# Kernel tuning notes

Hardware: AMD Instinct MI355X
Metric: run time of the kernel (lower is better)

## Reference

```python
import jax, jax.numpy as jnp
import numpy as np

N_NODES = 50000
N_EDGES = 800000
HID = 128
OUT = 10
N_LAYERS = 3
N_GRAPHS = 64
BN_EPS = 1e-5


def setup_inputs() -> dict:
    key = jax.random.key(0)
    ks = jax.random.split(key, 12)
    x = jax.random.normal(ks[0], (N_NODES, HID), dtype=jnp.float32)
    edge_index = jax.random.randint(ks[1], (2, N_EDGES), 0, N_NODES)
    batch = jnp.sort(jax.random.randint(ks[2], (N_NODES,), 0, N_GRAPHS))
    s = 1.0 / np.sqrt(HID)
    # per-layer MLP params (in_channels == hidden_channels so all layers stack)
    W1s = jax.random.uniform(ks[3], (N_LAYERS, HID, HID), jnp.float32, -s, s)
    b1s = jax.random.uniform(ks[4], (N_LAYERS, HID), jnp.float32, -s, s)
    W2s = jax.random.uniform(ks[5], (N_LAYERS, HID, HID), jnp.float32, -s, s)
    b2s = jax.random.uniform(ks[6], (N_LAYERS, HID), jnp.float32, -s, s)
    gammas = jnp.ones((N_LAYERS, HID), jnp.float32)
    betas = jnp.zeros((N_LAYERS, HID), jnp.float32)
    Wlin = jax.random.uniform(ks[7], (HID, OUT), jnp.float32, -s, s)
    blin = jax.random.uniform(ks[8], (OUT,), jnp.float32, -s, s)
    return {"x": x, "W1s": W1s, "b1s": b1s, "W2s": W2s, "b2s": b2s,
            "gammas": gammas, "betas": betas, "Wlin": Wlin, "blin": blin,
            "edge_index": edge_index, "batch": batch}


def reference(x, W1s, b1s, W2s, b2s, gammas, betas, Wlin, blin, edge_index, batch):
    src, dst = edge_index[0], edge_index[1]
    n = x.shape[0]
    for l in range(N_LAYERS):
        # GINConv (eps=0): h_i = MLP(x_i + sum_{j->i} x_j)
        agg = jax.ops.segment_sum(x[src], dst, num_segments=n)  # [N, HID]
        h = x + agg
        h = jnp.maximum(h @ W1s[l] + b1s[l], 0.0) @ W2s[l] + b2s[l]
        # BatchNorm1d (batch statistics)
        mean = jnp.mean(h, axis=0)
        var = jnp.var(h, axis=0)
        h = (h - mean) * jax.lax.rsqrt(var + BN_EPS) * gammas[l] + betas[l]
        x = jnp.maximum(h, 0.0)  # ReLU; dropout is identity in eval mode
    # global_add_pool over graphs
    g = jax.ops.segment_sum(x, batch, num_segments=N_GRAPHS)  # [G, HID]
    return g @ Wlin + blin
```

## Files before the change

kernel.cpp:

```cpp
#include <hip/hip_runtime.h>

#define N_NODES 50000
#define N_EDGES 800000
#define HID 128
#define OUTC 10
#define N_GRAPHS 64
#define BN_EPS 1e-5f

#define MLP_BLOCKS (N_NODES / 16)

#define NB 196
#define BCAP 5632
#define EPB 2048
#define NBLK_A ((N_EDGES + EPB - 1) / EPB)

typedef __attribute__((ext_vector_type(8))) short short8_t;
typedef __attribute__((ext_vector_type(4))) float f32x4;

__device__ __forceinline__ unsigned short f2bf(float f) {
    unsigned u = __float_as_uint(f);
    u += 0x7FFFu + ((u >> 16) & 1u);
    return (unsigned short)(u >> 16);
}
__device__ __forceinline__ float bf2f(unsigned short s) {
    return __uint_as_float(((unsigned)s) << 16);
}
__device__ __forceinline__ float2 bfp2f(unsigned v) {
    float2 r;
    r.x = __uint_as_float(v << 16);
    r.y = __uint_as_float(v & 0xFFFF0000u);
    return r;
}

__global__ __launch_bounds__(256) void k_bucket(const int* __restrict__ src,
                                                const int* __restrict__ dst,
                                                int* __restrict__ bucketCnt,
                                                unsigned* __restrict__ ebuf) {
    __shared__ int cnt[NB];
    __shared__ int base[NB];
    int t = threadIdx.x;
    for (int i = t; i < NB; i += 256) cnt[i] = 0;
    __syncthreads();
    int e0 = blockIdx.x * EPB;
    int e1 = e0 + EPB; if (e1 > N_EDGES) e1 = N_EDGES;
    for (int e = e0 + t; e < e1; e += 256)
        atomicAdd(&cnt[dst[e] >> 8], 1);
    __syncthreads();
    for (int i = t; i < NB; i += 256) {
        int c = cnt[i];
        base[i] = c ? atomicAdd(&bucketCnt[i], c) : 0;
        cnt[i] = 0;
    }
    __syncthreads();
    for (int e = e0 + t; e < e1; e += 256) {
        int d = dst[e];
        int s = src[e];
        int b = d >> 8;
        int r = atomicAdd(&cnt[b], 1);
        ebuf[(size_t)b * BCAP + base[b] + r] = ((unsigned)(d & 255) << 16) | (unsigned)s;
    }
}

__global__ __launch_bounds__(256) void k_bsort(const int* __restrict__ bucketCnt,
                                               const unsigned* __restrict__ ebuf,
                                               unsigned short* __restrict__ srcSorted,
                                               int* __restrict__ estart,
                                               int* __restrict__ eend) {
    __shared__ int cnt[256];
    __shared__ int sh[256];
    __shared__ int pos[256];
    int b = blockIdx.x;
    int t = threadIdx.x;
    int n = bucketCnt[b];
    int bBase = b * BCAP;
    const unsigned* eb = ebuf + (size_t)bBase;
    cnt[t] = 0;
    __syncthreads();
    for (int i = t; i < n; i += 256) atomicAdd(&cnt[eb[i] >> 16], 1);
    __syncthreads();
    int v = cnt[t];
    sh[t] = v;
    __syncthreads();
    for (int off = 1; off < 256; off <<= 1) {
        int x = sh[t];
        if (t >= off) x += sh[t - off];
        __syncthreads();
        sh[t] = x;
        __syncthreads();
    }
    int excl = sh[t] - v;
    pos[t] = excl;
    int node = b * 256 + t;
    if (node < N_NODES) {
        estart[node] = bBase + excl;
        eend[node] = bBase + excl + v;
    }
    __syncthreads();
    for (int i = t; i < n; i += 256) {
        unsigned pe = eb[i];
        int dl = pe >> 16;
        int p = atomicAdd(&pos[dl], 1);
        srcSorted[bBase + p] = (unsigned short)(pe & 0xFFFFu);
    }
}

#define X2BF_ITEMS (N_NODES * HID / 8)
__global__ void k_prep(const float* __restrict__ x, const float* __restrict__ W1s,
                       const float* __restrict__ W2s,
                       unsigned short* __restrict__ xbf, unsigned short* __restrict__ Wp) {
    int gid = blockIdx.x * 256 + threadIdx.x;
    if (gid < X2BF_ITEMS) {
        const float4* p = (const float4*)&x[(size_t)gid * 8];
        float4 a = p[0], b = p[1];
        short8_t o = { (short)f2bf(a.x), (short)f2bf(a.y), (short)f2bf(a.z), (short)f2bf(a.w),
                       (short)f2bf(b.x), (short)f2bf(b.y), (short)f2bf(b.z), (short)f2bf(b.w) };
        *(short8_t*)&xbf[(size_t)gid * 8] = o;
    } else {
        int idx = gid - X2BF_ITEMS;
        if (idx >= 6 * 2048) return;
        int mat = idx >> 11;
        int rem = idx & 2047;
        int lane = rem & 63;
        int ks = (rem >> 6) & 3;
        int nt = rem >> 8;
        int l = mat >> 1;
        const float* W = (mat & 1) ? (W2s + (size_t)l * HID * HID) : (W1s + (size_t)l * HID * HID);
        int n = nt * 16 + (lane & 15);
        int k0 = ks * 32 + (lane >> 4) * 8;
        short8_t o;
#pragma unroll
        for (int j = 0; j < 8; j++) o[j] = (short)f2bf(W[(size_t)(k0 + j) * HID + n]);
        *(short8_t*)&Wp[(size_t)idx * 8] = o;
    }
}

#define MPITCH 136

template <bool BN>
__global__ __launch_bounds__(256) void k_aggmlp(const unsigned short* __restrict__ X,
                                                const float* __restrict__ sc,
                                                const int* __restrict__ estart,
                                                const int* __restrict__ eend,
                                                const unsigned short* __restrict__ srcSorted,
                                                const unsigned short* __restrict__ W1p,
                                                const float* __restrict__ b1,
                                                const unsigned short* __restrict__ W2p,
                                                const float* __restrict__ b2,
                                                unsigned short* __restrict__ hbf,
                                                float* __restrict__ bnpart) {
    __shared__ __align__(16) unsigned short As[16 * MPITCH];
    __shared__ __align__(16) unsigned short Ts[16 * MPITCH];

    int tid = threadIdx.x;
    int wave = tid >> 6;
    int lane = tid & 63;
    int lrow = lane & 15;
    int quad = lane >> 4;
    int half = lane >> 5;
    int hl = lane & 31;
    int hq = hl >> 4;
    int rowBase = blockIdx.x * 16;
    int col0 = lrow * 8;

    float scv[8], shv[8];
    if (BN) {
#pragma unroll
        for (int j = 0; j < 8; j++) { scv[j] = sc[col0 + j]; shv[j] = sc[HID + col0 + j]; }
    }

    for (int pr = 0; pr < 2; pr++) {
        int tr = wave * 4 + pr * 2 + half;
        int node = rowBase + tr;
        float acc[8];
        {
            short8_t ov = *(const short8_t*)&X[(size_t)node * HID + col0];
            uint4 uu = *(uint4*)&ov;
            float2 p0 = bfp2f(uu.x), p1 = bfp2f(uu.y), p2 = bfp2f(uu.z), p3 = bfp2f(uu.w);
            float f[8] = { p0.x, p0.y, p1.x, p1.y, p2.x, p2.y, p3.x, p3.y };
#pragma unroll
            for (int j = 0; j < 8; j++) {
                float v = BN ? fmaxf(f[j] * scv[j] + shv[j], 0.f) : f[j];
                acc[j] = (hq == 0) ? v : 0.f;
            }
        }

        int e0 = estart[node];
        int deg = eend[node] - e0;

        for (int base = 0; base < deg; base += 16) {
            int cnt = deg - base; if (cnt > 16) cnt = 16;
            int ipos = base + (hl & 15); if (ipos >= deg) ipos = deg - 1;
            int myidx = (int)srcSorted[e0 + ipos];

            short8_t v[8];
#pragma unroll
            for (int u = 0; u < 8; u++) {
                int slot = u * 2 + hq;
                int sl = slot < cnt ? slot : cnt - 1;
                int ridx = __shfl(myidx, (half << 5) + sl);
                v[u] = *(const short8_t*)&X[(size_t)ridx * HID + col0];
            }
#pragma unroll
            for (int u = 0; u < 8; u++) {
                int slot = u * 2 + hq;
                if (slot < cnt) {
                    uint4 uu = *(uint4*)&v[u];
                    float2 p0 = bfp2f(uu.x), p1 = bfp2f(uu.y), p2 = bfp2f(uu.z), p3 = bfp2f(uu.w);
                    float f[8] = { p0.x, p0.y, p1.x, p1.y, p2.x, p2.y, p3.x, p3.y };
#pragma unroll
                    for (int j = 0; j < 8; j++)
                        acc[j] += BN ? fmaxf(f[j] * scv[j] + shv[j], 0.f) : f[j];
                }
            }
        }

#pragma unroll
        for (int j = 0; j < 8; j++) acc[j] += __shfl_xor(acc[j], 16);
        if (hq == 0) {
            short8_t o;
#pragma unroll
            for (int j = 0; j < 8; j++) o[j] = (short)f2bf(acc[j]);
            *(short8_t*)&As[tr * MPITCH + col0] = o;
        }
    }
    __syncthreads();

    int t0 = wave * 2;
    short8_t a0f = *(const short8_t*)&As[lrow * MPITCH + 0 * 32 + quad * 8];
    short8_t a1f = *(const short8_t*)&As[lrow * MPITCH + 1 * 32 + quad * 8];
    short8_t a2f = *(const short8_t*)&As[lrow * MPITCH + 2 * 32 + quad * 8];
    short8_t a3f = *(const short8_t*)&As[lrow * MPITCH + 3 * 32 + quad * 8];

    f32x4 acc1[2];
#pragma unroll
    for (int ti = 0; ti < 2; ti++) {
        int t = t0 + ti;
        f32x4 a = (f32x4){ 0.f, 0.f, 0.f, 0.f };
        short8_t b0 = *(const short8_t*)&W1p[(size_t)((t * 4 + 0) * 64 + lane) * 8];
        short8_t b1_ = *(const short8_t*)&W1p[(size_t)((t * 4 + 1) * 64 + lane) * 8];
        short8_t b2_ = *(const short8_t*)&W1p[(size_t)((t * 4 + 2) * 64 + lane) * 8];
        short8_t b3 = *(const short8_t*)&W1p[(size_t)((t * 4 + 3) * 64 + lane) * 8];
        a = __builtin_amdgcn_mfma_f32_16x16x32_bf16(a0f, b0, a, 0, 0, 0);
        a = __builtin_amdgcn_mfma_f32_16x16x32_bf16(a1f, b1_, a, 0, 0, 0);
        a = __builtin_amdgcn_mfma_f32_16x16x32_bf16(a2f, b2_, a, 0, 0, 0);
        a = __builtin_amdgcn_mfma_f32_16x16x32_bf16(a3f, b3, a, 0, 0, 0);
        acc1[ti] = a;
    }

#pragma unroll
    for (int ti = 0; ti < 2; ti++) {
        int col = (t0 + ti) * 16 + lrow;
        float bb = b1[col];
#pragma unroll
        for (int r = 0; r < 4; r++) {
            float v = fmaxf(acc1[ti][r] + bb, 0.f);
            Ts[(quad * 4 + r) * MPITCH + col] = f2bf(v);
        }
    }
    __syncthreads();

    short8_t t0f = *(const short8_t*)&Ts[lrow * MPITCH + 0 * 32 + quad * 8];
    short8_t t1f = *(const short8_t*)&Ts[lrow * MPITCH + 1 * 32 + quad * 8];
    short8_t t2f = *(const short8_t*)&Ts[lrow * MPITCH + 2 * 32 + quad * 8];
    short8_t t3f = *(const short8_t*)&Ts[lrow * MPITCH + 3 * 32 + quad * 8];

    f32x4 acc2[2];
#pragma unroll
    for (int ti = 0; ti < 2; ti++) {
        int t = t0 + ti;
        f32x4 a = (f32x4){ 0.f, 0.f, 0.f, 0.f };
        short8_t b0 = *(const short8_t*)&W2p[(size_t)((t * 4 + 0) * 64 + lane) * 8];
        short8_t b1_ = *(const short8_t*)&W2p[(size_t)((t * 4 + 1) * 64 + lane) * 8];
        short8_t b2_ = *(const short8_t*)&W2p[(size_t)((t * 4 + 2) * 64 + lane) * 8];
        short8_t b3 = *(const short8_t*)&W2p[(size_t)((t * 4 + 3) * 64 + lane) * 8];
        a = __builtin_amdgcn_mfma_f32_16x16x32_bf16(t0f, b0, a, 0, 0, 0);
        a = __builtin_amdgcn_mfma_f32_16x16x32_bf16(t1f, b1_, a, 0, 0, 0);
        a = __builtin_amdgcn_mfma_f32_16x16x32_bf16(t2f, b2_, a, 0, 0, 0);
        a = __builtin_amdgcn_mfma_f32_16x16x32_bf16(t3f, b3, a, 0, 0, 0);
        acc2[ti] = a;
    }

#pragma unroll
    for (int ti = 0; ti < 2; ti++) {
        int t = t0 + ti;
        int col = t * 16 + lrow;
        float bb = b2[col];
        float p1 = 0.f, p2 = 0.f;
#pragma unroll
        for (int r = 0; r < 4; r++) {
            unsigned short bv = f2bf(acc2[ti][r] + bb);
            float vr = bf2f(bv);
            p1 += vr; p2 += vr * vr;
            As[(quad * 4 + r) * MPITCH + col] = bv;
        }
        p1 += __shfl_xor(p1, 16); p1 += __shfl_xor(p1, 32);
        p2 += __shfl_xor(p2, 16); p2 += __shfl_xor(p2, 32);
        if (quad == 0) {
            float* bp = bnpart + (size_t)blockIdx.x * 256;
            bp[t * 16 + lrow] = p1;
            bp[128 + t * 16 + lrow] = p2;
        }
    }
    __syncthreads();

    {
        int r = tid >> 4;
        int c8 = (tid & 15) * 8;
        *(short8_t*)&hbf[(size_t)(rowBase + r) * HID + c8] =
            *(const short8_t*)&As[r * MPITCH + c8];
    }
}

__global__ void k_bnred(const float* __restrict__ bnpart, float* __restrict__ bnred2) {
    float acc = 0.f;
    for (int r = blockIdx.x; r < MLP_BLOCKS; r += 64)
        acc += bnpart[(size_t)r * 256 + threadIdx.x];
    bnred2[blockIdx.x * 256 + threadIdx.x] = acc;
}

__global__ void k_bnscale(const float* __restrict__ bnred2, const float* __restrict__ gamma,
                          const float* __restrict__ beta, float* __restrict__ sc) {
    __shared__ float tot[256];
    int t = threadIdx.x;
    float a = 0.f;
    for (int j = 0; j < 64; j++) a += bnred2[j * 256 + t];
    tot[t] = a;
    __syncthreads();
    if (t < HID) {
        float mean = tot[t] * (1.0f / N_NODES);
        float var = tot[HID + t] * (1.0f / N_NODES) - mean * mean;
        float s = gamma[t] * rsqrtf(var + BN_EPS);
        sc[t] = s;
        sc[HID + t] = beta[t] - mean * s;
    }
}

#define POOL_CHUNK 512
__global__ void k_pool(const unsigned short* __restrict__ X, const float* __restrict__ sc,
                       const int* __restrict__ batch, float* __restrict__ g) {
    int lane = threadIdx.x & 31;
    int rg = threadIdx.x >> 5;
    int c = lane * 4;
    float4 s = *(const float4*)&sc[c];
    float4 b = *(const float4*)&sc[HID + c];
    int base = blockIdx.x * POOL_CHUNK;
    int end = base + POOL_CHUNK;
    if (end > N_NODES) end = N_NODES;
    float a0 = 0.f, a1 = 0.f, a2 = 0.f, a3 = 0.f;
    int cur = -1;
    for (int r = base + rg; r < end; r += 8) {
        int bb = batch[r];
        if (bb != cur) {
            if (cur >= 0) {
                atomicAdd(&g[cur * HID + c + 0], a0);
                atomicAdd(&g[cur * HID + c + 1], a1);
                atomicAdd(&g[cur * HID + c + 2], a2);
                atomicAdd(&g[cur * HID + c + 3], a3);
            }
            cur = bb;
            a0 = a1 = a2 = a3 = 0.f;
        }
        ushort4 v = *(const ushort4*)&X[(size_t)r * HID + c];
        a0 += fmaxf(bf2f(v.x) * s.x + b.x, 0.f);
        a1 += fmaxf(bf2f(v.y) * s.y + b.y, 0.f);
        a2 += fmaxf(bf2f(v.z) * s.z + b.z, 0.f);
        a3 += fmaxf(bf2f(v.w) * s.w + b.w, 0.f);
    }
    if (cur >= 0) {
        atomicAdd(&g[cur * HID + c + 0], a0);
        atomicAdd(&g[cur * HID + c + 1], a1);
        atomicAdd(&g[cur * HID + c + 2], a2);
        atomicAdd(&g[cur * HID + c + 3], a3);
    }
}

__global__ void k_final(const float* __restrict__ g, const float* __restrict__ Wlin,
                        const float* __restrict__ blin, float* __restrict__ out) {
    int o = blockIdx.x * 256 + threadIdx.x;
    if (o >= N_GRAPHS * OUTC) return;
    int gi = o / OUTC, c = o % OUTC;
    float s = blin[c];
    for (int k = 0; k < HID; k++) s += g[gi * HID + k] * Wlin[k * OUTC + c];
    out[o] = s;
}

extern "C" void kernel_launch(void* const* d_in, const int* in_sizes, int n_in,
                              void* d_out, int out_size, void* d_ws, size_t ws_size,
                              hipStream_t stream) {
    const float* x      = (const float*)d_in[0];
    const float* W1s    = (const float*)d_in[1];
    const float* b1s    = (const float*)d_in[2];
    const float* W2s    = (const float*)d_in[3];
    const float* b2s    = (const float*)d_in[4];
    const float* gammas = (const float*)d_in[5];
    const float* betas  = (const float*)d_in[6];
    const float* Wlin   = (const float*)d_in[7];
    const float* blin   = (const float*)d_in[8];
    const int* edge_index = (const int*)d_in[9];
    const int* batch    = (const int*)d_in[10];
    float* out = (float*)d_out;

    const int* src = edge_index;
    const int* dst = edge_index + N_EDGES;

    char* w = (char*)d_ws;
    int* bucketCnt = (int*)w;        w += 256 * 4;
    unsigned* ebuf = (unsigned*)w;   w += (size_t)NB * BCAP * 4;
    unsigned short* srcSorted = (unsigned short*)w; w += (size_t)NB * BCAP * 2;
    int* estart    = (int*)w;        w += (size_t)N_NODES * 4;
    int* eend      = (int*)w;        w += (size_t)N_NODES * 4;
    unsigned short* Xbf = (unsigned short*)w; w += (size_t)N_NODES * HID * 2;
    unsigned short* HA  = (unsigned short*)w; w += (size_t)N_NODES * HID * 2;
    unsigned short* HB  = (unsigned short*)w; w += (size_t)N_NODES * HID * 2;
    unsigned short* Wp  = (unsigned short*)w; w += (size_t)6 * 2048 * 8 * 2;
    float* bnpart = (float*)w; w += (size_t)MLP_BLOCKS * 256 * 4;
    float* bnred2 = (float*)w; w += (size_t)64 * 256 * 4;
    float* bnsc   = (float*)w; w += 2 * HID * 4;
    float* g      = (float*)w; w += (size_t)N_GRAPHS * HID * 4;

    hipMemsetAsync(bucketCnt, 0, 256 * 4, stream);
    hipMemsetAsync(g, 0, (size_t)N_GRAPHS * HID * 4, stream);

    k_bucket<<<NBLK_A, 256, 0, stream>>>(src, dst, bucketCnt, ebuf);
    k_bsort<<<NB, 256, 0, stream>>>(bucketCnt, ebuf, srcSorted, estart, eend);
    k_prep<<<(X2BF_ITEMS + 6 * 2048 + 255) / 256, 256, 0, stream>>>(x, W1s, W2s, Xbf, Wp);

    const unsigned short* in0 = Xbf;
    unsigned short* outs[3] = { HA, HB, HA };
    for (int l = 0; l < 3; l++) {
        const unsigned short* xin = (l == 0) ? in0 : outs[l - 1];
        if (l == 0)
            k_aggmlp<false><<<MLP_BLOCKS, 256, 0, stream>>>(
                xin, nullptr, estart, eend, srcSorted,
                Wp + (size_t)(l * 2 + 0) * 16384, b1s + (size_t)l * HID,
                Wp + (size_t)(l * 2 + 1) * 16384, b2s + (size_t)l * HID, outs[l], bnpart);
        else
            k_aggmlp<true><<<MLP_BLOCKS, 256, 0, stream>>>(
                xin, bnsc, estart, eend, srcSorted,
                Wp + (size_t)(l * 2 + 0) * 16384, b1s + (size_t)l * HID,
                Wp + (size_t)(l * 2 + 1) * 16384, b2s + (size_t)l * HID, outs[l], bnpart);
        k_bnred<<<64, 256, 0, stream>>>(bnpart, bnred2);
        k_bnscale<<<1, 256, 0, stream>>>(bnred2, gammas + (size_t)l * HID,
                                         betas + (size_t)l * HID, bnsc);
    }

    k_pool<<<(N_NODES + POOL_CHUNK - 1) / POOL_CHUNK, 256, 0, stream>>>(outs[2], bnsc, batch, g);
    k_final<<<(N_GRAPHS * OUTC + 255) / 256, 256, 0, stream>>>(g, Wlin, blin, out);
}
```

Measured before the change: 334.7 us.

## Fuse bucket and prep kernels, accumulate BN partials atomically into 64 slots

Merges the edge-bucketing and bf16 conversion kernels into one launch by splitting the grid, so both run concurrently. BatchNorm partial sums are now atomically added into 64 striped slots instead of one slot per block, which removes the separate reduction kernel. The scale kernel also clears those slots and the pooling buffer, replacing one memset. This cuts several launches per forward pass at the cost of float atomic contention and non-deterministic summation order.

```diff
diff --git a/kernel.cpp b/kernel.cpp
--- a/kernel.cpp
+++ b/kernel.cpp
@@ -14,6 +14,10 @@
 #define EPB 2048
 #define NBLK_A ((N_EDGES + EPB - 1) / EPB)
 
+#define X2BF_ITEMS (N_NODES * HID / 8)
+#define PREP_ITEMS (X2BF_ITEMS + 6 * 2048)
+#define NBLK_PREP ((PREP_ITEMS + 255) / 256)
+
 typedef __attribute__((ext_vector_type(8))) short short8_t;
 typedef __attribute__((ext_vector_type(4))) float f32x4;
 
@@ -32,32 +36,64 @@
     return r;
 }
 
-__global__ __launch_bounds__(256) void k_bucket(const int* __restrict__ src,
-                                                const int* __restrict__ dst,
-                                                int* __restrict__ bucketCnt,
-                                                unsigned* __restrict__ ebuf) {
-    __shared__ int cnt[NB];
-    __shared__ int base[NB];
+__global__ __launch_bounds__(256) void k_bucketprep(const int* __restrict__ src,
+                                                    const int* __restrict__ dst,
+                                                    int* __restrict__ bucketCnt,
+                                                    unsigned* __restrict__ ebuf,
+                                                    const float* __restrict__ x,
+                                                    const float* __restrict__ W1s,
+                                                    const float* __restrict__ W2s,
+                                                    unsigned short* __restrict__ xbf,
+                                                    unsigned short* __restrict__ Wp) {
     int t = threadIdx.x;
-    for (int i = t; i < NB; i += 256) cnt[i] = 0;
-    __syncthreads();
-    int e0 = blockIdx.x * EPB;
-    int e1 = e0 + EPB; if (e1 > N_EDGES) e1 = N_EDGES;
-    for (int e = e0 + t; e < e1; e += 256)
-        atomicAdd(&cnt[dst[e] >> 8], 1);
-    __syncthreads();
-    for (int i = t; i < NB; i += 256) {
-        int c = cnt[i];
-        base[i] = c ? atomicAdd(&bucketCnt[i], c) : 0;
-        cnt[i] = 0;
-    }
-    __syncthreads();
-    for (int e = e0 + t; e < e1; e += 256) {
-        int d = dst[e];
-        int s = src[e];
-        int b = d >> 8;
-        int r = atomicAdd(&cnt[b], 1);
-        ebuf[(size_t)b * BCAP + base[b] + r] = ((unsigned)(d & 255) << 16) | (unsigned)s;
+    if (blockIdx.x < NBLK_A) {
+        __shared__ int cnt[NB];
+        __shared__ int base[NB];
+        for (int i = t; i < NB; i += 256) cnt[i] = 0;
+        __syncthreads();
+        int e0 = blockIdx.x * EPB;
+        int e1 = e0 + EPB; if (e1 > N_EDGES) e1 = N_EDGES;
+        for (int e = e0 + t; e < e1; e += 256)
+            atomicAdd(&cnt[dst[e] >> 8], 1);
+        __syncthreads();
+        for (int i = t; i < NB; i += 256) {
+            int c = cnt[i];
+            base[i] = c ? atomicAdd(&bucketCnt[i], c) : 0;
+            cnt[i] = 0;
+        }
+        __syncthreads();
+        for (int e = e0 + t; e < e1; e += 256) {
+            int d = dst[e];
+            int s = src[e];
+            int b = d >> 8;
+            int r = atomicAdd(&cnt[b], 1);
+            ebuf[(size_t)b * BCAP + base[b] + r] = ((unsigned)(d & 255) << 16) | (unsigned)s;
+        }
+    } else {
+        int gid = (blockIdx.x - NBLK_A) * 256 + t;
+        if (gid < X2BF_ITEMS) {
+            const float4* p = (const float4*)&x[(size_t)gid * 8];
+            float4 a = p[0], b = p[1];
+            short8_t o = { (short)f2bf(a.x), (short)f2bf(a.y), (short)f2bf(a.z), (short)f2bf(a.w),
+                           (short)f2bf(b.x), (short)f2bf(b.y), (short)f2bf(b.z), (short)f2bf(b.w) };
+            *(short8_t*)&xbf[(size_t)gid * 8] = o;
+        } else {
+            int idx = gid - X2BF_ITEMS;
+            if (idx >= 6 * 2048) return;
+            int mat = idx >> 11;
+            int rem = idx & 2047;
+            int lane = rem & 63;
+            int ks = (rem >> 6) & 3;
+            int nt = rem >> 8;
+            int l = mat >> 1;
+            const float* W = (mat & 1) ? (W2s + (size_t)l * HID * HID) : (W1s + (size_t)l * HID * HID);
+            int n = nt * 16 + (lane & 15);
+            int k0 = ks * 32 + (lane >> 4) * 8;
+            short8_t o;
+#pragma unroll
+            for (int j = 0; j < 8; j++) o[j] = (short)f2bf(W[(size_t)(k0 + j) * HID + n]);
+            *(short8_t*)&Wp[(size_t)idx * 8] = o;
+        }
     }
 }
 
@@ -104,36 +140,6 @@
     }
 }
 
-#define X2BF_ITEMS (N_NODES * HID / 8)
-__global__ void k_prep(const float* __restrict__ x, const float* __restrict__ W1s,
-                       const float* __restrict__ W2s,
-                       unsigned short* __restrict__ xbf, unsigned short* __restrict__ Wp) {
-    int gid = blockIdx.x * 256 + threadIdx.x;
-    if (gid < X2BF_ITEMS) {
-        const float4* p = (const float4*)&x[(size_t)gid * 8];
-        float4 a = p[0], b = p[1];
-        short8_t o = { (short)f2bf(a.x), (short)f2bf(a.y), (short)f2bf(a.z), (short)f2bf(a.w),
-                       (short)f2bf(b.x), (short)f2bf(b.y), (short)f2bf(b.z), (short)f2bf(b.w) };
-        *(short8_t*)&xbf[(size_t)gid * 8] = o;
-    } else {
-        int idx = gid - X2BF_ITEMS;
-        if (idx >= 6 * 2048) return;
-        int mat = idx >> 11;
-        int rem = idx & 2047;
-        int lane = rem & 63;
-        int ks = (rem >> 6) & 3;
-        int nt = rem >> 8;
-        int l = mat >> 1;
-        const float* W = (mat & 1) ? (W2s + (size_t)l * HID * HID) : (W1s + (size_t)l * HID * HID);
-        int n = nt * 16 + (lane & 15);
-        int k0 = ks * 32 + (lane >> 4) * 8;
-        short8_t o;
-#pragma unroll
-        for (int j = 0; j < 8; j++) o[j] = (short)f2bf(W[(size_t)(k0 + j) * HID + n]);
-        *(short8_t*)&Wp[(size_t)idx * 8] = o;
-    }
-}
-
 #define MPITCH 136
 
 template <bool BN>
@@ -296,9 +302,9 @@
         p1 += __shfl_xor(p1, 16); p1 += __shfl_xor(p1, 32);
         p2 += __shfl_xor(p2, 16); p2 += __shfl_xor(p2, 32);
         if (quad == 0) {
-            float* bp = bnpart + (size_t)blockIdx.x * 256;
-            bp[t * 16 + lrow] = p1;
-            bp[128 + t * 16 + lrow] = p2;
+            float* bp = bnpart + (size_t)(blockIdx.x & 63) * 256;
+            atomicAdd(&bp[col], p1);
+            atomicAdd(&bp[128 + col], p2);
         }
     }
     __syncthreads();
@@ -311,20 +317,16 @@
     }
 }
 
-__global__ void k_bnred(const float* __restrict__ bnpart, float* __restrict__ bnred2) {
-    float acc = 0.f;
-    for (int r = blockIdx.x; r < MLP_BLOCKS; r += 64)
-        acc += bnpart[(size_t)r * 256 + threadIdx.x];
-    bnred2[blockIdx.x * 256 + threadIdx.x] = acc;
-}
-
-__global__ void k_bnscale(const float* __restrict__ bnred2, const float* __restrict__ gamma,
-                          const float* __restrict__ beta, float* __restrict__ sc) {
+__global__ void k_bnscale2(float* __restrict__ bnpart, const float* __restrict__ gamma,
+                           const float* __restrict__ beta, float* __restrict__ sc,
+                           float* __restrict__ g) {
     __shared__ float tot[256];
     int t = threadIdx.x;
     float a = 0.f;
-    for (int j = 0; j < 64; j++) a += bnred2[j * 256 + t];
+    for (int j = 0; j < 64; j++) a += bnpart[j * 256 + t];
     tot[t] = a;
+    for (int j = 0; j < 64; j++) bnpart[j * 256 + t] = 0.f;
+    for (int i = t; i < N_GRAPHS * HID; i += 256) g[i] = 0.f;
     __syncthreads();
     if (t < HID) {
         float mean = tot[t] * (1.0f / N_NODES);
@@ -405,6 +407,7 @@
 
     char* w = (char*)d_ws;
     int* bucketCnt = (int*)w;        w += 256 * 4;
+    float* bnpart  = (float*)w;      w += (size_t)64 * 256 * 4;
     unsigned* ebuf = (unsigned*)w;   w += (size_t)NB * BCAP * 4;
     unsigned short* srcSorted = (unsigned short*)w; w += (size_t)NB * BCAP * 2;
     int* estart    = (int*)w;        w += (size_t)N_NODES * 4;
@@ -413,17 +416,14 @@
     unsigned short* HA  = (unsigned short*)w; w += (size_t)N_NODES * HID * 2;
     unsigned short* HB  = (unsigned short*)w; w += (size_t)N_NODES * HID * 2;
     unsigned short* Wp  = (unsigned short*)w; w += (size_t)6 * 2048 * 8 * 2;
-    float* bnpart = (float*)w; w += (size_t)MLP_BLOCKS * 256 * 4;
-    float* bnred2 = (float*)w; w += (size_t)64 * 256 * 4;
     float* bnsc   = (float*)w; w += 2 * HID * 4;
     float* g      = (float*)w; w += (size_t)N_GRAPHS * HID * 4;
 
-    hipMemsetAsync(bucketCnt, 0, 256 * 4, stream);
-    hipMemsetAsync(g, 0, (size_t)N_GRAPHS * HID * 4, stream);
-
-    k_bucket<<<NBLK_A, 256, 0, stream>>>(src, dst, bucketCnt, ebuf);
+    hipMemsetAsync(bucketCnt, 0, 256 * 4 + 64 * 256 * 4, stream);
+
+    k_bucketprep<<<NBLK_A + NBLK_PREP, 256, 0, stream>>>(src, dst, bucketCnt, ebuf,
+                                                         x, W1s, W2s, Xbf, Wp);
     k_bsort<<<NB, 256, 0, stream>>>(bucketCnt, ebuf, srcSorted, estart, eend);
-    k_prep<<<(X2BF_ITEMS + 6 * 2048 + 255) / 256, 256, 0, stream>>>(x, W1s, W2s, Xbf, Wp);
 
     const unsigned short* in0 = Xbf;
     unsigned short* outs[3] = { HA, HB, HA };
@@ -439,9 +439,8 @@
                 xin, bnsc, estart, eend, srcSorted,
                 Wp + (size_t)(l * 2 + 0) * 16384, b1s + (size_t)l * HID,
                 Wp + (size_t)(l * 2 + 1) * 16384, b2s + (size_t)l * HID, outs[l], bnpart);
-        k_bnred<<<64, 256, 0, stream>>>(bnpart, bnred2);
-        k_bnscale<<<1, 256, 0, stream>>>(bnred2, gammas + (size_t)l * HID,
-                                         betas + (size_t)l * HID, bnsc);
+        k_bnscale2<<<1, 256, 0, stream>>>(bnpart, gammas + (size_t)l * HID,
+                                          betas + (size_t)l * HID, bnsc, g);
     }
 
     k_pool<<<(N_NODES + POOL_CHUNK - 1) / POOL_CHUNK, 256, 0, stream>>>(outs[2], bnsc, batch, g);
```

After: 289.3 us. -13.5%, faster.
